# Kernel tuning notes

Hardware: AMD Instinct MI355X
Metric: run time of the kernel (lower is better)

## Reference

```python
import jax, jax.numpy as jnp
import numpy as np

TAU = 100.0
DT = 20.0
ALPHA = DT / TAU  # 0.2, fixed buffer (train_alpha=False)


def setup_inputs() -> dict:
    key = jax.random.key(0)
    ks = jax.random.split(key, 12)
    T, B, I, H = 64, 32, 128, 256

    def lin(kw, out_f, in_f):
        bound = 1.0 / np.sqrt(in_f)
        kw1, kw2 = jax.random.split(kw)
        w = jax.random.uniform(kw1, (out_f, in_f), jnp.float32, -bound, bound)
        b = jax.random.uniform(kw2, (out_f,), jnp.float32, -bound, bound)
        return w, b

    w_i2h, b_i2h = lin(ks[0], H, I)
    w_h2h, b_h2h = lin(ks[1], H, H)
    w_i2c, b_i2c = lin(ks[2], H, I)
    w_c2c, b_c2c = lin(ks[3], H, H)
    w_c2t, b_c2t = lin(ks[4], H * H, H)
    x = jax.random.normal(ks[5], (T, B, I), jnp.float32)
    return {
        "input": x,
        "w_i2h": w_i2h, "b_i2h": b_i2h,
        "w_h2h": w_h2h, "b_h2h": b_h2h,
        "w_i2c": w_i2c, "b_i2c": b_i2c,
        "w_c2c": w_c2c, "b_c2c": b_c2c,
        "w_c2t": w_c2t, "b_c2t": b_c2t,
        "num_steps": 1,
    }


def reference(input, w_i2h, b_i2h, w_h2h, b_h2h, w_i2c, b_i2c,
              w_c2c, b_c2c, w_c2t, b_c2t, num_steps):
    H = w_i2h.shape[0]
    B = input.shape[1]
    a = jnp.float32(ALPHA)

    def recurrence(x, hidden, context):
        input_proj = x @ w_i2h.T + b_i2h                      # [B,H]
        tm = (context @ w_c2t.T + b_c2t).reshape(B, H, H)     # per-sample hypernet matrix
        transformed = jnp.einsum('bij,bj->bi', tm, input_proj)
        h_new = jax.nn.relu(context + transformed + hidden @ w_h2h.T + b_h2h)
        hidden = hidden * (1 - a) + h_new * a
        context_new = jax.nn.relu(context @ w_c2c.T + b_c2c + x @ w_i2c.T + b_i2c)
        context = context * (1 - a) + context_new * a
        hidden = transformed  # NOTE: faithful to source, overwrites leaky update
        return hidden, context

    def step(carry, x):
        hidden, context = carry
        for _ in range(num_steps):
            hidden, context = recurrence(x, hidden, context)
        return (hidden, context), hidden

    h0 = jnp.zeros((B, H), input.dtype)
    c0 = jnp.zeros((B, H), input.dtype)
    (hidden, context), output = jax.lax.scan(step, (h0, c0), input)
    return output, hidden, context
```

## Files before the change

kernel.cpp:

```cpp
#include <hip/hip_runtime.h>

#define TT 64
#define BB 32
#define II 128
#define HH 256
#define MM (TT*BB)

typedef __bf16  bf16x8  __attribute__((ext_vector_type(8)));
typedef float   f32x16  __attribute__((ext_vector_type(16)));
typedef _Float16 half2v __attribute__((ext_vector_type(2)));

__device__ __forceinline__ float bf2f(unsigned short u) {
    union { unsigned int i; float f; } v; v.i = ((unsigned int)u) << 16; return v.f;
}
__device__ __forceinline__ unsigned short f2bf(float f) {
    union { float f; unsigned int i; } v; v.f = f;
    unsigned int r = v.i + 0x7fffu + ((v.i >> 16) & 1u);
    return (unsigned short)(r >> 16);
}

struct F8 { float v[8]; };
__device__ __forceinline__ F8 load8(const void* base, int idx, int isf32) {
    F8 r;
    if (isf32) {
        const float4* p = (const float4*)((const float*)base + idx);
        float4 a = p[0], b = p[1];
        r.v[0]=a.x; r.v[1]=a.y; r.v[2]=a.z; r.v[3]=a.w;
        r.v[4]=b.x; r.v[5]=b.y; r.v[6]=b.z; r.v[7]=b.w;
    } else {
        uint4 u = *(const uint4*)((const unsigned short*)base + idx);
        const unsigned short* p = (const unsigned short*)&u;
#pragma unroll
        for (int j = 0; j < 8; ++j) r.v[j] = bf2f(p[j]);
    }
    return r;
}
__device__ __forceinline__ float load1(const void* base, int idx, int isf32) {
    return isf32 ? ((const float*)base)[idx]
                 : bf2f(((const unsigned short*)base)[idx]);
}

__device__ __forceinline__ float fdot2f(half2v a, half2v b, float c) {
#if __has_builtin(__builtin_amdgcn_fdot2)
    return __builtin_amdgcn_fdot2(a, b, c, false);
#else
    return c + (float)a.x*(float)b.x + (float)a.y*(float)b.y;
#endif
}

__global__ __launch_bounds__(256) void k0_sniff(
    const unsigned short* __restrict__ x, int* __restrict__ flag)
{
    __shared__ int cnt;
    if (threadIdx.x == 0) cnt = 0;
    __syncthreads();
    int c = 0;
    for (int i = threadIdx.x; i < 8192; i += 256) {
        unsigned int e = (x[i] >> 7) & 0xFFu;
        if (e >= 0xC0u) ++c;
    }
    atomicAdd(&cnt, c);
    __syncthreads();
    if (threadIdx.x == 0) flag[0] = (cnt > 16) ? 1 : 0;
}

__global__ __launch_bounds__(256) void k1_proj(
    const void* __restrict__ x,
    const void* __restrict__ w_i2h,
    const void* __restrict__ b_i2h,
    const void* __restrict__ w_i2c,
    const void* __restrict__ b_i2c,
    const int* __restrict__ flagp,
    unsigned short* __restrict__ ip,
    float* __restrict__ cin)
{
    const int isf32 = *flagp;
    const int tid = threadIdx.x;
    const int h = tid;
    const int mbase = blockIdx.x * 32;
    __shared__ __align__(16) _Float16 xs[32][II];

    half2v w1[II/2], w2[II/2];
#pragma unroll
    for (int c8 = 0; c8 < II/8; ++c8) {
        F8 f1 = load8(w_i2h, h*II + c8*8, isf32);
        F8 f2 = load8(w_i2c, h*II + c8*8, isf32);
#pragma unroll
        for (int j = 0; j < 4; ++j) {
            half2v a; a.x = (_Float16)f1.v[2*j]; a.y = (_Float16)f1.v[2*j+1];
            half2v b; b.x = (_Float16)f2.v[2*j]; b.y = (_Float16)f2.v[2*j+1];
            w1[c8*4 + j] = a;
            w2[c8*4 + j] = b;
        }
    }
    const float bb1 = load1(b_i2h, h, isf32);
    const float bb2 = load1(b_i2c, h, isf32);

    for (int u = tid; u < 32*II; u += 256)
        xs[u >> 7][u & (II-1)] = (_Float16)load1(x, (mbase + (u >> 7))*II + (u & (II-1)), isf32);
    __syncthreads();

    for (int mm = 0; mm < 32; ++mm) {
        const half2v* xv = (const half2v*)xs[mm];
        float a0=0,a1=0,a2=0,a3=0, c0=0,c1=0,c2=0,c3=0;
#pragma unroll
        for (int r = 0; r < II/2; r += 4) {
            half2v x0 = xv[r], x1 = xv[r+1], x2 = xv[r+2], x3 = xv[r+3];
            a0 = fdot2f(w1[r],   x0, a0);
            a1 = fdot2f(w1[r+1], x1, a1);
            a2 = fdot2f(w1[r+2], x2, a2);
            a3 = fdot2f(w1[r+3], x3, a3);
            c0 = fdot2f(w2[r],   x0, c0);
            c1 = fdot2f(w2[r+1], x1, c1);
            c2 = fdot2f(w2[r+2], x2, c2);
            c3 = fdot2f(w2[r+3], x3, c3);
        }
        ip[(mbase+mm)*HH + h]  = f2bf(((a0+a1)+(a2+a3)) + bb1);
        cin[(mbase+mm)*HH + h] = ((c0+c1)+(c2+c3)) + bb2;
    }
}

__global__ __launch_bounds__(256) void k2_ctx(
    const void* __restrict__ w_c2c,
    const void* __restrict__ b_c2c,
    const float* __restrict__ cin,
    const int* __restrict__ ns_ptr,
    const int* __restrict__ flagp,
    unsigned short* __restrict__ ctx_hist,
    void* __restrict__ out_base)
{
    const int isf32 = *flagp;
    const int b = blockIdx.x;
    const int h = threadIdx.x;
    const int ns = max(1, *ns_ptr);

    __shared__ __align__(16) _Float16 cs[2][HH];

    half2v w[HH/2];
#pragma unroll
    for (int c8 = 0; c8 < HH/8; ++c8) {
        F8 f = load8(w_c2c, h*HH + c8*8, isf32);
#pragma unroll
        for (int j = 0; j < 4; ++j) {
            half2v hv;
            hv.x = (_Float16)f.v[2*j];
            hv.y = (_Float16)f.v[2*j+1];
            w[c8*4 + j] = hv;
        }
    }
    const float bcc = load1(b_c2c, h, isf32);
    float ctxv = 0.0f;
    cs[0][h] = (_Float16)0.0f;
    __syncthreads();
    int cur = 0;

    for (int t = 0; t < TT; ++t) {
        const float cinv = cin[(t*BB + b)*HH + h];
        for (int s = 0; s < ns; ++s) {
            if (s == ns-1) ctx_hist[(t*BB + b)*HH + h] = f2bf(ctxv);
            float p0=0,p1=0,p2=0,p3=0;
            const float4* cp4 = (const float4*)cs[cur];
#pragma unroll
            for (int r4 = 0; r4 < HH/8; ++r4) {
                float4 blob = cp4[r4];
                const half2v* c2 = (const half2v*)&blob;
                p0 = fdot2f(w[r4*4+0], c2[0], p0);
                p1 = fdot2f(w[r4*4+1], c2[1], p1);
                p2 = fdot2f(w[r4*4+2], c2[2], p2);
                p3 = fdot2f(w[r4*4+3], c2[3], p3);
            }
            float cnew = fmaxf(((p0+p1)+(p2+p3)) + bcc + cinv, 0.0f);
            ctxv = 0.8f*ctxv + 0.2f*cnew;
            cs[cur^1][h] = (_Float16)ctxv;
            cur ^= 1;
            __syncthreads();
        }
    }
    const int cofs = MM*HH + BB*HH + b*HH + h;
    if (isf32) ((float*)out_base)[cofs] = ctxv;
    else       ((unsigned short*)out_base)[cofs] = f2bf(ctxv);
}

__global__ __launch_bounds__(512, 1) void k3_main(
    const unsigned short* __restrict__ ctx_hist,
    const void* __restrict__ wc,
    const void* __restrict__ bc,
    const unsigned short* __restrict__ ip,
    const int* __restrict__ flagp,
    float* __restrict__ outT)
{
    extern __shared__ __align__(16) unsigned char lds[];
    unsigned short* Bs = (unsigned short*)lds;
    unsigned short* As = (unsigned short*)(lds + 131072);
    float*          part = (float*)(lds + 131072);

    const int isf32 = *flagp;
    const int tid  = threadIdx.x;
    const int lane = tid & 63;
    const int wave = tid >> 6;
    const int i    = blockIdx.x;
    const int mh   = wave & 3;
    const int jh   = wave >> 2;
    const int l31  = lane & 31;
    const int lhi  = lane >> 5;

    float bcv[4];
#pragma unroll
    for (int n = 0; n < 4; ++n)
        bcv[n] = load1(bc, i*HH + jh*128 + n*32 + l31, isf32);

#pragma unroll
    for (int p = 0; p < 16; ++p) {
        int u = tid + p*512;
        int row = u >> 5, cu = u & 31;
        F8 f = load8(wc, (i*HH + row)*HH + cu*8, isf32);
        unsigned short tmp[8];
#pragma unroll
        for (int j = 0; j < 8; ++j) tmp[j] = f2bf(f.v[j]);
        *(uint4*)(Bs + row*256 + ((cu ^ (row & 7)) << 3)) = *(const uint4*)tmp;
    }

    uint4 areg[4];
#pragma unroll
    for (int p = 0; p < 4; ++p) {
        int u = tid + p*512;
        int row = u >> 3, cu = u & 7;
        areg[p] = *(const uint4*)(ctx_hist + row*HH + cu*8);
    }

    for (int mc = 0; mc < 8; ++mc) {
        const int m0 = mc * 256;

        f32x16 acc[2][4];
#pragma unroll
        for (int a = 0; a < 2; ++a)
#pragma unroll
            for (int n = 0; n < 4; ++n)
#pragma unroll
                for (int r = 0; r < 16; ++r) acc[a][n][r] = 0.0f;

#pragma unroll
        for (int kc = 0; kc < 4; ++kc) {
            __syncthreads();
#pragma unroll
            for (int p = 0; p < 4; ++p) {
                int u = tid + p*512;
                int row = u >> 3, cu = u & 7;
                *(uint4*)(As + row*64 + ((cu ^ (row & 7)) << 3)) = areg[p];
            }
            __syncthreads();
            {
                int nmc = mc, nkc = kc + 1;
                if (nkc == 4) { nkc = 0; nmc = mc + 1; }
                if (nmc < 8) {
                    const unsigned short* src = ctx_hist + (nmc*256)*HH + nkc*64;
#pragma unroll
                    for (int p = 0; p < 4; ++p) {
                        int u = tid + p*512;
                        int row = u >> 3, cu = u & 7;
                        areg[p] = *(const uint4*)(src + row*HH + cu*8);
                    }
                }
            }
#pragma unroll
            for (int ks = 0; ks < 4; ++ks) {
                const int cA = ks*2 + lhi;
                const int ra0 = mh*64 + l31;
                const int ra1 = ra0 + 32;
                bf16x8 a0 = *(const bf16x8*)(As + ra0*64 + ((cA ^ (ra0 & 7)) << 3));
                bf16x8 a1 = *(const bf16x8*)(As + ra1*64 + ((cA ^ (ra1 & 7)) << 3));
                const int cB = kc*8 + ks*2 + lhi;
                const int rb0 = jh*128 +       l31;
                const int rb1 = jh*128 + 32  + l31;
                const int rb2 = jh*128 + 64  + l31;
                const int rb3 = jh*128 + 96  + l31;
                bf16x8 b0 = *(const bf16x8*)(Bs + rb0*256 + ((cB ^ (rb0 & 7)) << 3));
                bf16x8 b1 = *(const bf16x8*)(Bs + rb1*256 + ((cB ^ (rb1 & 7)) << 3));
                bf16x8 b2 = *(const bf16x8*)(Bs + rb2*256 + ((cB ^ (rb2 & 7)) << 3));
                bf16x8 b3 = *(const bf16x8*)(Bs + rb3*256 + ((cB ^ (rb3 & 7)) << 3));
                acc[0][0] = __builtin_amdgcn_mfma_f32_32x32x16_bf16(a0, b0, acc[0][0], 0, 0, 0);
                acc[0][1] = __builtin_amdgcn_mfma_f32_32x32x16_bf16(a0, b1, acc[0][1], 0, 0, 0);
                acc[0][2] = __builtin_amdgcn_mfma_f32_32x32x16_bf16(a0, b2, acc[0][2], 0, 0, 0);
                acc[0][3] = __builtin_amdgcn_mfma_f32_32x32x16_bf16(a0, b3, acc[0][3], 0, 0, 0);
                acc[1][0] = __builtin_amdgcn_mfma_f32_32x32x16_bf16(a1, b0, acc[1][0], 0, 0, 0);
                acc[1][1] = __builtin_amdgcn_mfma_f32_32x32x16_bf16(a1, b1, acc[1][1], 0, 0, 0);
                acc[1][2] = __builtin_amdgcn_mfma_f32_32x32x16_bf16(a1, b2, acc[1][2], 0, 0, 0);
                acc[1][3] = __builtin_amdgcn_mfma_f32_32x32x16_bf16(a1, b3, acc[1][3], 0, 0, 0);
            }
        }

        __syncthreads();
#pragma unroll
        for (int a = 0; a < 2; ++a) {
#pragma unroll
            for (int r = 0; r < 16; ++r) {
                const int rl = (r & 3) + 8*(r >> 2) + 4*lhi;
                const int gm = m0 + mh*64 + a*32 + rl;
                const unsigned short* ipr = ip + gm*HH + jh*128 + l31;
                float p = 0.0f;
#pragma unroll
                for (int n = 0; n < 4; ++n)
                    p = fmaf(acc[a][n][r] + bcv[n], bf2f(ipr[n*32]), p);
                p += __shfl_xor(p, 1);
                p += __shfl_xor(p, 2);
                p += __shfl_xor(p, 4);
                p += __shfl_xor(p, 8);
                p += __shfl_xor(p, 16);
                if (l31 == rl) part[jh*256 + mh*64 + a*32 + rl] = p;
            }
        }
        __syncthreads();
        if (tid < 256)
            outT[(size_t)i*MM + m0 + tid] = part[tid] + part[256 + tid];
    }
}

__global__ __launch_bounds__(256) void k4_tr(
    const float* __restrict__ outT,
    const int* __restrict__ flagp,
    void* __restrict__ out)
{
    const int isf32 = *flagp;
    __shared__ float tile[64][65];
    const int m0 = blockIdx.x * 64, i0 = blockIdx.y * 64;
    const int tm = threadIdx.x & 63, tq = threadIdx.x >> 6;
#pragma unroll
    for (int rep = 0; rep < 16; ++rep) {
        int il = tq + rep*4;
        tile[il][tm] = outT[(size_t)(i0 + il)*MM + m0 + tm];
    }
    __syncthreads();
#pragma unroll
    for (int rep = 0; rep < 16; ++rep) {
        int ml = tq + rep*4;
        int ii = tm;
        float v = tile[ii][ml];
        int mg = m0 + ml, ig = i0 + ii;
        if (isf32) {
            float* o = (float*)out;
            o[(size_t)mg*HH + ig] = v;
            if (mg >= MM - BB) o[(size_t)MM*HH + (mg - (MM-BB))*HH + ig] = v;
        } else {
            unsigned short* o = (unsigned short*)out;
            unsigned short b = f2bf(v);
            o[(size_t)mg*HH + ig] = b;
            if (mg >= MM - BB) o[(size_t)MM*HH + (mg - (MM-BB))*HH + ig] = b;
        }
    }
}

extern "C" void kernel_launch(void* const* d_in, const int* in_sizes, int n_in,
                              void* d_out, int out_size, void* d_ws, size_t ws_size,
                              hipStream_t stream) {
    const void* x     = d_in[0];
    const void* w_i2h = d_in[1];
    const void* b_i2h = d_in[2];
    const void* w_i2c = d_in[5];
    const void* b_i2c = d_in[6];
    const void* w_c2c = d_in[7];
    const void* b_c2c = d_in[8];
    const void* w_c2t = d_in[9];
    const void* b_c2t = d_in[10];
    const int* ns     = (const int*)d_in[11];

    unsigned short* ip  = (unsigned short*)d_ws;
    unsigned short* ch  = (unsigned short*)((char*)d_ws + (size_t)MM*HH*2);
    float* cin          = (float*)((char*)d_ws + (size_t)MM*HH*4);
    int* flag           = (int*)((char*)d_ws + (size_t)MM*HH*8);
    float* outT         = (float*)((char*)d_ws + (size_t)MM*HH*8 + 1024);

    (void)hipFuncSetAttribute((const void*)k3_main,
                              hipFuncAttributeMaxDynamicSharedMemorySize, 163840);

    k0_sniff<<<1, 256, 0, stream>>>((const unsigned short*)x, flag);
    k1_proj<<<64, 256, 0, stream>>>(x, w_i2h, b_i2h, w_i2c, b_i2c, flag, ip, cin);
    k2_ctx<<<BB, 256, 0, stream>>>(w_c2c, b_c2c, cin, ns, flag, ch, d_out);
    k3_main<<<256, 512, 163840, stream>>>(ch, w_c2t, b_c2t, ip, flag, outT);
    k4_tr<<<dim3(32, 4), 256, 0, stream>>>(outT, flag, d_out);
}
```

Baseline: 405.6 us.

## Split context recurrence K across two thread halves, restage epilogue through LDS

The context recurrence kernel now runs 512 threads per batch, with each half computing a partial dot product over half of the hidden dimension. The partials are reduced through shared memory at the cost of an extra barrier per step. The main MFMA kernel changes its LDS swizzle to a column-major unit layout for A and B. Its epilogue now writes bf16 accumulators to LDS and computes the row dot products with coalesced loads and full-wave shuffles, which adds bf16 rounding of the hypernet matrix. The projection kernel preloads x into registers as float4.

After: 564.1 us. 39.1% more time.

```diff
diff --git a/kernel.cpp b/kernel.cpp
--- a/kernel.cpp
+++ b/kernel.cpp
@@ -101,26 +101,29 @@
     __syncthreads();
 
     for (int mm = 0; mm < 32; ++mm) {
-        const half2v* xv = (const half2v*)xs[mm];
+        const float4* xv4 = (const float4*)xs[mm];
+        float4 blob[16];
+#pragma unroll
+        for (int r = 0; r < 16; ++r) blob[r] = xv4[r];
         float a0=0,a1=0,a2=0,a3=0, c0=0,c1=0,c2=0,c3=0;
 #pragma unroll
-        for (int r = 0; r < II/2; r += 4) {
-            half2v x0 = xv[r], x1 = xv[r+1], x2 = xv[r+2], x3 = xv[r+3];
-            a0 = fdot2f(w1[r],   x0, a0);
-            a1 = fdot2f(w1[r+1], x1, a1);
-            a2 = fdot2f(w1[r+2], x2, a2);
-            a3 = fdot2f(w1[r+3], x3, a3);
-            c0 = fdot2f(w2[r],   x0, c0);
-            c1 = fdot2f(w2[r+1], x1, c1);
-            c2 = fdot2f(w2[r+2], x2, c2);
-            c3 = fdot2f(w2[r+3], x3, c3);
+        for (int r = 0; r < 16; ++r) {
+            const half2v* xc = (const half2v*)&blob[r];
+            a0 = fdot2f(w1[r*4+0], xc[0], a0);
+            a1 = fdot2f(w1[r*4+1], xc[1], a1);
+            a2 = fdot2f(w1[r*4+2], xc[2], a2);
+            a3 = fdot2f(w1[r*4+3], xc[3], a3);
+            c0 = fdot2f(w2[r*4+0], xc[0], c0);
+            c1 = fdot2f(w2[r*4+1], xc[1], c1);
+            c2 = fdot2f(w2[r*4+2], xc[2], c2);
+            c3 = fdot2f(w2[r*4+3], xc[3], c3);
         }
         ip[(mbase+mm)*HH + h]  = f2bf(((a0+a1)+(a2+a3)) + bb1);
         cin[(mbase+mm)*HH + h] = ((c0+c1)+(c2+c3)) + bb2;
     }
 }
 
-__global__ __launch_bounds__(256) void k2_ctx(
+__global__ __launch_bounds__(512) void k2_ctx(
     const void* __restrict__ w_c2c,
     const void* __restrict__ b_c2c,
     const float* __restrict__ cin,
@@ -131,15 +134,18 @@
 {
     const int isf32 = *flagp;
     const int b = blockIdx.x;
-    const int h = threadIdx.x;
+    const int tid = threadIdx.x;
+    const int h  = tid & 255;
+    const int kh = tid >> 8;
     const int ns = max(1, *ns_ptr);
 
     __shared__ __align__(16) _Float16 cs[2][HH];
-
-    half2v w[HH/2];
-#pragma unroll
-    for (int c8 = 0; c8 < HH/8; ++c8) {
-        F8 f = load8(w_c2c, h*HH + c8*8, isf32);
+    __shared__ __align__(16) float part[2][HH];
+
+    half2v w[64];
+#pragma unroll
+    for (int c8 = 0; c8 < 16; ++c8) {
+        F8 f = load8(w_c2c, h*HH + kh*128 + c8*8, isf32);
 #pragma unroll
         for (int j = 0; j < 4; ++j) {
             half2v hv;
@@ -148,37 +154,45 @@
             w[c8*4 + j] = hv;
         }
     }
-    const float bcc = load1(b_c2c, h, isf32);
+    const float bcc = (kh == 0) ? load1(b_c2c, h, isf32) : 0.0f;
     float ctxv = 0.0f;
-    cs[0][h] = (_Float16)0.0f;
+    if (kh == 0) cs[0][h] = (_Float16)0.0f;
     __syncthreads();
     int cur = 0;
 
     for (int t = 0; t < TT; ++t) {
-        const float cinv = cin[(t*BB + b)*HH + h];
+        const float cinv = (kh == 0) ? cin[(t*BB + b)*HH + h] : 0.0f;
         for (int s = 0; s < ns; ++s) {
-            if (s == ns-1) ctx_hist[(t*BB + b)*HH + h] = f2bf(ctxv);
+            if (kh == 0 && s == ns-1) ctx_hist[(t*BB + b)*HH + h] = f2bf(ctxv);
+            float4 blob[16];
+            const float4* cp4 = (const float4*)cs[cur] + kh*16;
+#pragma unroll
+            for (int r = 0; r < 16; ++r) blob[r] = cp4[r];
             float p0=0,p1=0,p2=0,p3=0;
-            const float4* cp4 = (const float4*)cs[cur];
-#pragma unroll
-            for (int r4 = 0; r4 < HH/8; ++r4) {
-                float4 blob = cp4[r4];
-                const half2v* c2 = (const half2v*)&blob;
-                p0 = fdot2f(w[r4*4+0], c2[0], p0);
-                p1 = fdot2f(w[r4*4+1], c2[1], p1);
-                p2 = fdot2f(w[r4*4+2], c2[2], p2);
-                p3 = fdot2f(w[r4*4+3], c2[3], p3);
-            }
-            float cnew = fmaxf(((p0+p1)+(p2+p3)) + bcc + cinv, 0.0f);
-            ctxv = 0.8f*ctxv + 0.2f*cnew;
-            cs[cur^1][h] = (_Float16)ctxv;
+#pragma unroll
+            for (int r = 0; r < 16; ++r) {
+                const half2v* c2 = (const half2v*)&blob[r];
+                p0 = fdot2f(w[r*4+0], c2[0], p0);
+                p1 = fdot2f(w[r*4+1], c2[1], p1);
+                p2 = fdot2f(w[r*4+2], c2[2], p2);
+                p3 = fdot2f(w[r*4+3], c2[3], p3);
+            }
+            part[kh][h] = ((p0+p1)+(p2+p3));
+            __syncthreads();
+            if (kh == 0) {
+                float cnew = fmaxf(part[0][h] + part[1][h] + bcc + cinv, 0.0f);
+                ctxv = 0.8f*ctxv + 0.2f*cnew;
+                cs[cur^1][h] = (_Float16)ctxv;
+            }
             cur ^= 1;
             __syncthreads();
         }
     }
-    const int cofs = MM*HH + BB*HH + b*HH + h;
-    if (isf32) ((float*)out_base)[cofs] = ctxv;
-    else       ((unsigned short*)out_base)[cofs] = f2bf(ctxv);
+    if (kh == 0) {
+        const int cofs = MM*HH + BB*HH + b*HH + h;
+        if (isf32) ((float*)out_base)[cofs] = ctxv;
+        else       ((unsigned short*)out_base)[cofs] = f2bf(ctxv);
+    }
 }
 
 __global__ __launch_bounds__(512, 1) void k3_main(
@@ -192,7 +206,7 @@
     extern __shared__ __align__(16) unsigned char lds[];
     unsigned short* Bs = (unsigned short*)lds;
     unsigned short* As = (unsigned short*)(lds + 131072);
-    float*          part = (float*)(lds + 131072);
+    unsigned short* TMh = As;
 
     const int isf32 = *flagp;
     const int tid  = threadIdx.x;
@@ -204,10 +218,10 @@
     const int l31  = lane & 31;
     const int lhi  = lane >> 5;
 
-    float bcv[4];
-#pragma unroll
-    for (int n = 0; n < 4; ++n)
-        bcv[n] = load1(bc, i*HH + jh*128 + n*32 + l31, isf32);
+    float bcl[4];
+#pragma unroll
+    for (int q = 0; q < 4; ++q)
+        bcl[q] = load1(bc, i*HH + 4*lane + q, isf32);
 
 #pragma unroll
     for (int p = 0; p < 16; ++p) {
@@ -217,7 +231,8 @@
         unsigned short tmp[8];
 #pragma unroll
         for (int j = 0; j < 8; ++j) tmp[j] = f2bf(f.v[j]);
-        *(uint4*)(Bs + row*256 + ((cu ^ (row & 7)) << 3)) = *(const uint4*)tmp;
+        int unit = cu*256 + (row & ~7) + ((row & 7) ^ (cu & 7));
+        *(uint4*)(Bs + unit*8) = *(const uint4*)tmp;
     }
 
     uint4 areg[4];
@@ -246,7 +261,8 @@
             for (int p = 0; p < 4; ++p) {
                 int u = tid + p*512;
                 int row = u >> 3, cu = u & 7;
-                *(uint4*)(As + row*64 + ((cu ^ (row & 7)) << 3)) = areg[p];
+                int unit = cu*256 + (row & ~7) + ((row & 7) ^ cu);
+                *(uint4*)(As + unit*8) = areg[p];
             }
             __syncthreads();
             {
@@ -267,17 +283,18 @@
                 const int cA = ks*2 + lhi;
                 const int ra0 = mh*64 + l31;
                 const int ra1 = ra0 + 32;
-                bf16x8 a0 = *(const bf16x8*)(As + ra0*64 + ((cA ^ (ra0 & 7)) << 3));
-                bf16x8 a1 = *(const bf16x8*)(As + ra1*64 + ((cA ^ (ra1 & 7)) << 3));
+                bf16x8 a0 = *(const bf16x8*)(As + (cA*256 + (ra0 & ~7) + ((ra0 & 7) ^ cA))*8);
+                bf16x8 a1 = *(const bf16x8*)(As + (cA*256 + (ra1 & ~7) + ((ra1 & 7) ^ cA))*8);
                 const int cB = kc*8 + ks*2 + lhi;
+                const int cx = cB & 7;
                 const int rb0 = jh*128 +       l31;
                 const int rb1 = jh*128 + 32  + l31;
                 const int rb2 = jh*128 + 64  + l31;
                 const int rb3 = jh*128 + 96  + l31;
-                bf16x8 b0 = *(const bf16x8*)(Bs + rb0*256 + ((cB ^ (rb0 & 7)) << 3));
-                bf16x8 b1 = *(const bf16x8*)(Bs + rb1*256 + ((cB ^ (rb1 & 7)) << 3));
-                bf16x8 b2 = *(const bf16x8*)(Bs + rb2*256 + ((cB ^ (rb2 & 7)) << 3));
-                bf16x8 b3 = *(const bf16x8*)(Bs + rb3*256 + ((cB ^ (rb3 & 7)) << 3));
+                bf16x8 b0 = *(const bf16x8*)(Bs + (cB*256 + (rb0 & ~7) + ((rb0 & 7) ^ cx))*8);
+                bf16x8 b1 = *(const bf16x8*)(Bs + (cB*256 + (rb1 & ~7) + ((rb1 & 7) ^ cx))*8);
+                bf16x8 b2 = *(const bf16x8*)(Bs + (cB*256 + (rb2 & ~7) + ((rb2 & 7) ^ cx))*8);
+                bf16x8 b3 = *(const bf16x8*)(Bs + (cB*256 + (rb3 & ~7) + ((rb3 & 7) ^ cx))*8);
                 acc[0][0] = __builtin_amdgcn_mfma_f32_32x32x16_bf16(a0, b0, acc[0][0], 0, 0, 0);
                 acc[0][1] = __builtin_amdgcn_mfma_f32_32x32x16_bf16(a0, b1, acc[0][1], 0, 0, 0);
                 acc[0][2] = __builtin_amdgcn_mfma_f32_32x32x16_bf16(a0, b2, acc[0][2], 0, 0, 0);
@@ -291,27 +308,43 @@
 
         __syncthreads();
 #pragma unroll
-        for (int a = 0; a < 2; ++a) {
-#pragma unroll
-            for (int r = 0; r < 16; ++r) {
-                const int rl = (r & 3) + 8*(r >> 2) + 4*lhi;
-                const int gm = m0 + mh*64 + a*32 + rl;
-                const unsigned short* ipr = ip + gm*HH + jh*128 + l31;
-                float p = 0.0f;
-#pragma unroll
-                for (int n = 0; n < 4; ++n)
-                    p = fmaf(acc[a][n][r] + bcv[n], bf2f(ipr[n*32]), p);
-                p += __shfl_xor(p, 1);
-                p += __shfl_xor(p, 2);
-                p += __shfl_xor(p, 4);
-                p += __shfl_xor(p, 8);
-                p += __shfl_xor(p, 16);
-                if (l31 == rl) part[jh*256 + mh*64 + a*32 + rl] = p;
-            }
-        }
-        __syncthreads();
-        if (tid < 256)
-            outT[(size_t)i*MM + m0 + tid] = part[tid] + part[256 + tid];
+        for (int ph = 0; ph < 4; ++ph) {
+            if (mh == ph) {
+#pragma unroll
+                for (int a = 0; a < 2; ++a)
+#pragma unroll
+                    for (int n = 0; n < 4; ++n) {
+                        const int col = jh*128 + n*32 + l31;
+#pragma unroll
+                        for (int r = 0; r < 16; ++r) {
+                            const int rowl = a*32 + (r & 3) + 8*(r >> 2) + 4*lhi;
+                            TMh[rowl*256 + col] = f2bf(acc[a][n][r]);
+                        }
+                    }
+            }
+            __syncthreads();
+#pragma unroll
+            for (int rep = 0; rep < 8; ++rep) {
+                const int rowg = wave*8 + rep;
+                const int g = m0 + ph*64 + rowg;
+                uint2 tm2 = *(const uint2*)(TMh + rowg*256 + 4*lane);
+                uint2 ip2 = *(const uint2*)(ip + g*HH + 4*lane);
+                const unsigned short* tp = (const unsigned short*)&tm2;
+                const unsigned short* pp = (const unsigned short*)&ip2;
+                float s = 0.0f;
+#pragma unroll
+                for (int q = 0; q < 4; ++q)
+                    s = fmaf(bf2f(tp[q]) + bcl[q], bf2f(pp[q]), s);
+                s += __shfl_xor(s, 1);
+                s += __shfl_xor(s, 2);
+                s += __shfl_xor(s, 4);
+                s += __shfl_xor(s, 8);
+                s += __shfl_xor(s, 16);
+                s += __shfl_xor(s, 32);
+                if (lane == rep) outT[(size_t)i*MM + g] = s;
+            }
+            __syncthreads();
+        }
     }
 }
 
@@ -374,7 +407,7 @@
 
     k0_sniff<<<1, 256, 0, stream>>>((const unsigned short*)x, flag);
     k1_proj<<<64, 256, 0, stream>>>(x, w_i2h, b_i2h, w_i2c, b_i2c, flag, ip, cin);
-    k2_ctx<<<BB, 256, 0, stream>>>(w_c2c, b_c2c, cin, ns, flag, ch, d_out);
+    k2_ctx<<<BB, 512, 0, stream>>>(w_c2c, b_c2c, cin, ns, flag, ch, d_out);
     k3_main<<<256, 512, 163840, stream>>>(ch, w_c2t, b_c2t, ip, flag, outT);
     k4_tr<<<dim3(32, 4), 256, 0, stream>>>(outT, flag, d_out);
 }
```
